# Kernel optimization log

Hardware: AMD Instinct MI355X
Metric: run time of the kernel (lower is better)

## Reference

```python
import jax, jax.numpy as jnp
import numpy as np

EPS = 1e-7  # K.epsilon()


def setup_inputs() -> dict:
    key = jax.random.key(0)
    k1, k2, k3, k4 = jax.random.split(key, 4)
    B, T, S = 512, 32, 2048  # batch, time_steps, seq_len
    inputs = jax.random.normal(k1, (B, T, S), dtype=jnp.float32)
    # Keras mask (float 0/1), same shape as inputs
    mask = (jax.random.uniform(k2, (B, T, S)) < 0.8).astype(jnp.float32)
    # 'uniform' keras initializer: U(-0.05, 0.05)
    W = jax.random.uniform(k3, (S, T, T), minval=-0.05, maxval=0.05, dtype=jnp.float32)
    b = jax.random.uniform(k4, (S, T), minval=-0.05, maxval=0.05, dtype=jnp.float32)
    return {"inputs": inputs, "mask": mask, "W": W, "b": b}


def reference(inputs, mask, W, b):
    # (B,T,S) -> (B,S,T), apply mask
    x = jnp.transpose(inputs, (0, 2, 1)) * jnp.transpose(mask, (0, 2, 1))
    # per-position matmul, batched over B and S (replaces the tf.scan over batch)
    z = jnp.einsum('bst,stu->bsu', x, W) + b  # (B,S,T)
    e = jnp.exp(jnp.tanh(z))
    att = e / (jnp.sum(e, axis=2, keepdims=True) + EPS)  # softmax-like over T
    return jnp.sum(att * x, axis=1)  # (B,T)
```

## Files before the change

### kernel.cpp

```cpp
#include <hip/hip_runtime.h>

#define EPS_K 1e-7f

typedef __attribute__((ext_vector_type(8)))  short          frag8;
typedef __attribute__((ext_vector_type(16))) float          accf16;
typedef __attribute__((ext_vector_type(4)))  unsigned short us4;

__device__ __forceinline__ unsigned f2bf(float f) {
  union { float f; unsigned u; } v; v.f = f;
  unsigned u = v.u;
  u += 0x7FFFu + ((u >> 16) & 1u);
  return u >> 16;
}
__device__ __forceinline__ float bf2f(unsigned short s) {
  union { unsigned u; float f; } v; v.u = ((unsigned)s) << 16;
  return v.f;
}
__device__ __forceinline__ unsigned pk_bf16(float lo, float hi) {
  return f2bf(lo) | (f2bf(hi) << 16);
}

__global__ __launch_bounds__(256) void wbf_prep(
    const float* __restrict__ Wt, unsigned short* __restrict__ Wbf)
{
  __shared__ unsigned short tile[32 * 33];
  const int s   = blockIdx.x;
  const int tid = threadIdx.x;
  {
    const int t  = tid >> 3;
    const int uc = tid & 7;
    const float4 v = *(const float4*)(Wt + s * 1024 + t * 32 + 4 * uc);
    tile[t * 33 + 4 * uc + 0] = (unsigned short)f2bf(v.x);
    tile[t * 33 + 4 * uc + 1] = (unsigned short)f2bf(v.y);
    tile[t * 33 + 4 * uc + 2] = (unsigned short)f2bf(v.z);
    tile[t * 33 + 4 * uc + 3] = (unsigned short)f2bf(v.w);
  }
  __syncthreads();
  {
    const int u  = tid >> 3;
    const int tc = tid & 7;
    uint2 d;
    d.x = (unsigned)tile[(4 * tc + 0) * 33 + u] | ((unsigned)tile[(4 * tc + 1) * 33 + u] << 16);
    d.y = (unsigned)tile[(4 * tc + 2) * 33 + u] | ((unsigned)tile[(4 * tc + 3) * 33 + u] << 16);
    *(uint2*)(Wbf + s * 1024 + u * 32 + 4 * tc) = d;
  }
}

template <bool WBF, bool USE_WS>
__global__ __launch_bounds__(512, 8) void attn_fused(
    const float* __restrict__ inp,
    const float* __restrict__ msk,
    const float* __restrict__ Wt,
    const unsigned short* __restrict__ Wbf,
    const float* __restrict__ bias,
    float* __restrict__ part,
    float* __restrict__ out)
{
  __shared__ unsigned short x_us[32 * 512];

  const int tid = threadIdx.x;
  const int st  = blockIdx.x >> 4;
  const int bg  = blockIdx.x & 15;
  const int s0  = st * 16;

  {
    const int sc = tid & 3;
    const int tb = (tid >> 2) & 3;
    const int b  = tid >> 4;
    const float* ip = inp + ((size_t)(bg * 32 + b) * 32 + 8 * tb) * 2048 + s0 + 4 * sc;
    const float* mp = msk + ((size_t)(bg * 32 + b) * 32 + 8 * tb) * 2048 + s0 + 4 * sc;
    unsigned c32[4][4];
    #pragma unroll
    for (int j2 = 0; j2 < 4; ++j2) {
      const float4 vi0 = *(const float4*)(ip + (2 * j2)     * 2048);
      const float4 vm0 = *(const float4*)(mp + (2 * j2)     * 2048);
      const float4 vi1 = *(const float4*)(ip + (2 * j2 + 1) * 2048);
      const float4 vm1 = *(const float4*)(mp + (2 * j2 + 1) * 2048);
      c32[0][j2] = pk_bf16(vi0.x * vm0.x, vi1.x * vm1.x);
      c32[1][j2] = pk_bf16(vi0.y * vm0.y, vi1.y * vm1.y);
      c32[2][j2] = pk_bf16(vi0.z * vm0.z, vi1.z * vm1.z);
      c32[3][j2] = pk_bf16(vi0.w * vm0.w, vi1.w * vm1.w);
    }
    #pragma unroll
    for (int w = 0; w < 4; ++w) {
      const int L = tb * 16 + 4 * sc + w;
      unsigned* dst = (unsigned*)(x_us + b * 512 + ((L ^ (b & 7)) * 8));
      *(uint4*)dst = make_uint4(c32[w][0], c32[w][1], c32[w][2], c32[w][3]);
    }
  }
  __syncthreads();

  const int lane = tid & 63;
  const int wv   = tid >> 6;
  const int n    = lane & 31;
  const int h    = lane >> 5;
  const int nx   = n & 7;

  float O[16];
  #pragma unroll
  for (int r = 0; r < 16; ++r) O[r] = 0.f;

  #pragma unroll
  for (int si = 0; si < 2; ++si) {
    const int sl = wv * 2 + si;
    const int s  = s0 + sl;

    frag8 a1, a2;
    if (WBF) {
      const unsigned short* wp = Wbf + s * 1024 + n * 32 + 8 * h;
      a1 = *(const frag8*)(wp);
      a2 = *(const frag8*)(wp + 16);
    } else {
      const float* Wp = Wt + s * 1024;
      #pragma unroll
      for (int j = 0; j < 8; ++j) {
        const int t1 = 8 * h + j;
        a1[j] = (short)f2bf(Wp[t1 * 32 + n]);
        a2[j] = (short)f2bf(Wp[(t1 + 16) * 32 + n]);
      }
    }

    const frag8 b1 = *(const frag8*)(x_us + n * 512 + (((h      * 16 + sl) ^ nx) * 8));
    const frag8 b2 = *(const frag8*)(x_us + n * 512 + ((((h + 2) * 16 + sl) ^ nx) * 8));

    accf16 acc;
    #pragma unroll
    for (int g = 0; g < 4; ++g) {
      const float4 bb = *(const float4*)(bias + s * 32 + 8 * g + 4 * h);
      acc[4 * g + 0] = bb.x; acc[4 * g + 1] = bb.y;
      acc[4 * g + 2] = bb.z; acc[4 * g + 3] = bb.w;
    }
    acc = __builtin_amdgcn_mfma_f32_32x32x16_bf16(a1, b1, acc, 0, 0, 0);
    acc = __builtin_amdgcn_mfma_f32_32x32x16_bf16(a2, b2, acc, 0, 0, 0);

    float e[16];
    float ps = 0.f;
    #pragma unroll
    for (int r = 0; r < 16; ++r) {
      const float z  = acc[r];
      const float e2 = __expf(2.f * z);
      const float th = 1.f - 2.f / (e2 + 1.f);
      e[r] = __expf(th);
      ps  += e[r];
    }
    const float tot = ps + __shfl_xor(ps, 32, 64);
    const float inv = 1.f / (tot + EPS_K);

    #pragma unroll
    for (int g = 0; g < 4; ++g) {
      const us4 xv = *(const us4*)(x_us + n * 512 + (((g * 16 + sl) ^ nx) * 8) + 4 * h);
      #pragma unroll
      for (int i = 0; i < 4; ++i)
        O[4 * g + i] += e[4 * g + i] * inv * bf2f(xv[i]);
    }
  }

  __syncthreads();
  float* red = (float*)x_us;
  #pragma unroll
  for (int r = 0; r < 16; ++r) {
    const int u = (r & 3) + 8 * (r >> 2) + 4 * h;
    red[wv * 1024 + n * 32 + (u ^ n)] = O[r];
  }
  __syncthreads();

  const int q0 = tid * 2;
  float2 v;
  #pragma unroll
  for (int i = 0; i < 2; ++i) {
    const int q = q0 + i;
    const int b = q >> 5, u = q & 31;
    float sum = 0.f;
    #pragma unroll
    for (int w = 0; w < 8; ++w) sum += red[w * 1024 + b * 32 + (u ^ b)];
    (&v.x)[i] = sum;
  }
  if (USE_WS) {
    *(float2*)(part + (size_t)st * 16384 + bg * 1024 + q0) = v;
  } else {
    float* op = out + bg * 1024 + q0;
    atomicAdd(op + 0, v.x);
    atomicAdd(op + 1, v.y);
  }
}

__global__ __launch_bounds__(256) void reduce_part(
    const float* __restrict__ part, float* __restrict__ out)
{
  const int f = blockIdx.x * 256 + threadIdx.x;
  float s = 0.f;
  #pragma unroll 8
  for (int st = 0; st < 128; ++st) s += part[(size_t)st * 16384 + f];
  out[f] = s;
}

extern "C" void kernel_launch(void* const* d_in, const int* in_sizes, int n_in,
                              void* d_out, int out_size, void* d_ws, size_t ws_size,
                              hipStream_t stream) {
  const float* inp  = (const float*)d_in[0];
  const float* msk  = (const float*)d_in[1];
  const float* Wt   = (const float*)d_in[2];
  const float* bias = (const float*)d_in[3];
  float* out = (float*)d_out;

  const size_t part_sz = (size_t)128 * 16384 * sizeof(float);
  const size_t wbf_sz  = (size_t)2048 * 1024 * sizeof(unsigned short);

  if (ws_size >= part_sz + wbf_sz) {
    float* part = (float*)d_ws;
    unsigned short* Wbf = (unsigned short*)((char*)d_ws + part_sz);
    wbf_prep<<<dim3(2048), dim3(256), 0, stream>>>(Wt, Wbf);
    attn_fused<true, true><<<dim3(2048), dim3(512), 0, stream>>>(
        inp, msk, Wt, Wbf, bias, part, out);
    reduce_part<<<dim3(64), dim3(256), 0, stream>>>(part, out);
  } else if (ws_size >= part_sz) {
    float* part = (float*)d_ws;
    attn_fused<false, true><<<dim3(2048), dim3(512), 0, stream>>>(
        inp, msk, Wt, nullptr, bias, part, out);
    reduce_part<<<dim3(64), dim3(256), 0, stream>>>(part, out);
  } else {
    (void)hipMemsetAsync(out, 0, (size_t)out_size * sizeof(float), stream);
    attn_fused<false, false><<<dim3(2048), dim3(512), 0, stream>>>(
        inp, msk, Wt, nullptr, bias, nullptr, out);
  }
}
```

Baseline: 335.2 us.

## Make attention kernel persistent over s-chunks with double-buffered LDS prefetch

Each block now handles 8 chunks of 8 sequence positions, strided by 256, instead of one 16-position chunk. Global loads for the next chunk are issued into registers while the current chunk's MFMA and softmax run, and a double-buffered LDS tile replaces the single-shot load. The grid shrinks to 512 blocks, and the partial-sum buffer and its reduction drop from 128 to 32 slices. Divides are swapped for hardware reciprocal, and launch bounds are relaxed to 4 blocks per CU. In exchange there is a strided access pattern across s, fewer blocks to cover latency, and slightly lower reciprocal accuracy.

New measurement: 395.0 us. +17.8%, slower.

```diff
diff --git a/kernel.cpp b/kernel.cpp
--- a/kernel.cpp
+++ b/kernel.cpp
@@ -18,6 +18,9 @@
 }
 __device__ __forceinline__ unsigned pk_bf16(float lo, float hi) {
   return f2bf(lo) | (f2bf(hi) << 16);
+}
+__device__ __forceinline__ float rcp_f(float x) {
+  return __builtin_amdgcn_rcpf(x);
 }
 
 __global__ __launch_bounds__(256) void wbf_prep(
@@ -47,7 +50,7 @@
 }
 
 template <bool WBF, bool USE_WS>
-__global__ __launch_bounds__(512, 8) void attn_fused(
+__global__ __launch_bounds__(512, 4) void attn_fused(
     const float* __restrict__ inp,
     const float* __restrict__ msk,
     const float* __restrict__ Wt,
@@ -56,39 +59,48 @@
     float* __restrict__ part,
     float* __restrict__ out)
 {
-  __shared__ unsigned short x_us[32 * 512];
+  __shared__ unsigned short x_us[2][32 * 256];
 
   const int tid = threadIdx.x;
-  const int st  = blockIdx.x >> 4;
+  const int sq  = blockIdx.x >> 4;
   const int bg  = blockIdx.x & 15;
-  const int s0  = st * 16;
-
-  {
-    const int sc = tid & 3;
-    const int tb = (tid >> 2) & 3;
-    const int b  = tid >> 4;
-    const float* ip = inp + ((size_t)(bg * 32 + b) * 32 + 8 * tb) * 2048 + s0 + 4 * sc;
-    const float* mp = msk + ((size_t)(bg * 32 + b) * 32 + 8 * tb) * 2048 + s0 + 4 * sc;
-    unsigned c32[4][4];
-    #pragma unroll
-    for (int j2 = 0; j2 < 4; ++j2) {
-      const float4 vi0 = *(const float4*)(ip + (2 * j2)     * 2048);
-      const float4 vm0 = *(const float4*)(mp + (2 * j2)     * 2048);
-      const float4 vi1 = *(const float4*)(ip + (2 * j2 + 1) * 2048);
-      const float4 vm1 = *(const float4*)(mp + (2 * j2 + 1) * 2048);
-      c32[0][j2] = pk_bf16(vi0.x * vm0.x, vi1.x * vm1.x);
-      c32[1][j2] = pk_bf16(vi0.y * vm0.y, vi1.y * vm1.y);
-      c32[2][j2] = pk_bf16(vi0.z * vm0.z, vi1.z * vm1.z);
-      c32[3][j2] = pk_bf16(vi0.w * vm0.w, vi1.w * vm1.w);
-    }
-    #pragma unroll
-    for (int w = 0; w < 4; ++w) {
-      const int L = tb * 16 + 4 * sc + w;
-      unsigned* dst = (unsigned*)(x_us + b * 512 + ((L ^ (b & 7)) * 8));
-      *(uint4*)dst = make_uint4(c32[w][0], c32[w][1], c32[w][2], c32[w][3]);
-    }
-  }
-  __syncthreads();
+
+  const int b_s  = tid & 31;
+  const int sc_s = (tid >> 5) & 1;
+  const int tq_s = tid >> 6;
+  const float* ip0 = inp + ((size_t)(bg * 32 + b_s) * 32 + 4 * tq_s) * 2048 + sq * 8 + 4 * sc_s;
+  const float* mp0 = msk + ((size_t)(bg * 32 + b_s) * 32 + 4 * tq_s) * 2048 + sq * 8 + 4 * sc_s;
+
+  float4 vi0, vi1, vi2, vi3, vm0, vm1, vm2, vm3;
+
+#define STAGE_LOAD(k) do {                                                   \
+    const float* ip = ip0 + (k) * 256;                                       \
+    const float* mp = mp0 + (k) * 256;                                       \
+    vi0 = *(const float4*)(ip);          vm0 = *(const float4*)(mp);         \
+    vi1 = *(const float4*)(ip + 2048);   vm1 = *(const float4*)(mp + 2048);  \
+    vi2 = *(const float4*)(ip + 4096);   vm2 = *(const float4*)(mp + 4096);  \
+    vi3 = *(const float4*)(ip + 6144);   vm3 = *(const float4*)(mp + 6144);  \
+  } while (0)
+
+#define STAGE_WRITE(k) do {                                                  \
+    unsigned short* xb = &x_us[(k) & 1][0];                                  \
+    _Pragma("unroll")                                                        \
+    for (int w = 0; w < 4; ++w) {                                            \
+      const int L = (tq_s >> 1) * 8 + 4 * sc_s + w;                          \
+      uint2 d;                                                               \
+      d.x = pk_bf16(((const float*)&vi0)[w] * ((const float*)&vm0)[w],       \
+                    ((const float*)&vi1)[w] * ((const float*)&vm1)[w]);      \
+      d.y = pk_bf16(((const float*)&vi2)[w] * ((const float*)&vm2)[w],       \
+                    ((const float*)&vi3)[w] * ((const float*)&vm3)[w]);      \
+      *(uint2*)(xb + b_s * 256 + ((L ^ (b_s & 7)) * 8) + 4 * (tq_s & 1)) = d;\
+    }                                                                        \
+  } while (0)
+
+#define SYNC do {                                                            \
+    asm volatile("s_waitcnt lgkmcnt(0)" ::: "memory");                       \
+    __builtin_amdgcn_s_barrier();                                            \
+    asm volatile("" ::: "memory");                                           \
+  } while (0)
 
   const int lane = tid & 63;
   const int wv   = tid >> 6;
@@ -100,10 +112,15 @@
   #pragma unroll
   for (int r = 0; r < 16; ++r) O[r] = 0.f;
 
-  #pragma unroll
-  for (int si = 0; si < 2; ++si) {
-    const int sl = wv * 2 + si;
-    const int s  = s0 + sl;
+  STAGE_LOAD(0);
+  STAGE_WRITE(0);
+  STAGE_LOAD(1);
+  SYNC;
+
+  #pragma unroll
+  for (int k = 0; k < 8; ++k) {
+    const int s = k * 256 + sq * 8 + wv;
+    const unsigned short* xb = &x_us[k & 1][0];
 
     frag8 a1, a2;
     if (WBF) {
@@ -120,8 +137,8 @@
       }
     }
 
-    const frag8 b1 = *(const frag8*)(x_us + n * 512 + (((h      * 16 + sl) ^ nx) * 8));
-    const frag8 b2 = *(const frag8*)(x_us + n * 512 + ((((h + 2) * 16 + sl) ^ nx) * 8));
+    const frag8 b1 = *(const frag8*)(xb + n * 256 + (((h      * 8 + wv) ^ nx) * 8));
+    const frag8 b2 = *(const frag8*)(xb + n * 256 + ((((h + 2) * 8 + wv) ^ nx) * 8));
 
     accf16 acc;
     #pragma unroll
@@ -133,30 +150,35 @@
     acc = __builtin_amdgcn_mfma_f32_32x32x16_bf16(a1, b1, acc, 0, 0, 0);
     acc = __builtin_amdgcn_mfma_f32_32x32x16_bf16(a2, b2, acc, 0, 0, 0);
 
-    float e[16];
     float ps = 0.f;
     #pragma unroll
     for (int r = 0; r < 16; ++r) {
       const float z  = acc[r];
       const float e2 = __expf(2.f * z);
-      const float th = 1.f - 2.f / (e2 + 1.f);
-      e[r] = __expf(th);
-      ps  += e[r];
+      const float th = 1.f - 2.f * rcp_f(e2 + 1.f);
+      acc[r] = __expf(th);
+      ps    += acc[r];
     }
     const float tot = ps + __shfl_xor(ps, 32, 64);
-    const float inv = 1.f / (tot + EPS_K);
+    const float inv = rcp_f(tot + EPS_K);
 
     #pragma unroll
     for (int g = 0; g < 4; ++g) {
-      const us4 xv = *(const us4*)(x_us + n * 512 + (((g * 16 + sl) ^ nx) * 8) + 4 * h);
+      const us4 xv = *(const us4*)(xb + n * 256 + (((g * 8 + wv) ^ nx) * 8) + 4 * h);
       #pragma unroll
       for (int i = 0; i < 4; ++i)
-        O[4 * g + i] += e[4 * g + i] * inv * bf2f(xv[i]);
+        O[4 * g + i] += acc[4 * g + i] * inv * bf2f(xv[i]);
+    }
+
+    if (k < 7) {
+      STAGE_WRITE(k + 1);
+      if (k < 6) STAGE_LOAD(k + 2);
+      SYNC;
     }
   }
 
   __syncthreads();
-  float* red = (float*)x_us;
+  float* red = (float*)&x_us[0][0];
   #pragma unroll
   for (int r = 0; r < 16; ++r) {
     const int u = (r & 3) + 8 * (r >> 2) + 4 * h;
@@ -176,12 +198,16 @@
     (&v.x)[i] = sum;
   }
   if (USE_WS) {
-    *(float2*)(part + (size_t)st * 16384 + bg * 1024 + q0) = v;
+    *(float2*)(part + (size_t)sq * 16384 + bg * 1024 + q0) = v;
   } else {
     float* op = out + bg * 1024 + q0;
     atomicAdd(op + 0, v.x);
     atomicAdd(op + 1, v.y);
   }
+
+#undef STAGE_LOAD
+#undef STAGE_WRITE
+#undef SYNC
 }
 
 __global__ __launch_bounds__(256) void reduce_part(
@@ -190,7 +216,7 @@
   const int f = blockIdx.x * 256 + threadIdx.x;
   float s = 0.f;
   #pragma unroll 8
-  for (int st = 0; st < 128; ++st) s += part[(size_t)st * 16384 + f];
+  for (int sq = 0; sq < 32; ++sq) s += part[(size_t)sq * 16384 + f];
   out[f] = s;
 }
 
@@ -203,24 +229,24 @@
   const float* bias = (const float*)d_in[3];
   float* out = (float*)d_out;
 
-  const size_t part_sz = (size_t)128 * 16384 * sizeof(float);
+  const size_t part_sz = (size_t)32 * 16384 * sizeof(float);
   const size_t wbf_sz  = (size_t)2048 * 1024 * sizeof(unsigned short);
 
   if (ws_size >= part_sz + wbf_sz) {
     float* part = (float*)d_ws;
     unsigned short* Wbf = (unsigned short*)((char*)d_ws + part_sz);
     wbf_prep<<<dim3(2048), dim3(256), 0, stream>>>(Wt, Wbf);
-    attn_fused<true, true><<<dim3(2048), dim3(512), 0, stream>>>(
+    attn_fused<true, true><<<dim3(512), dim3(512), 0, stream>>>(
         inp, msk, Wt, Wbf, bias, part, out);
     reduce_part<<<dim3(64), dim3(256), 0, stream>>>(part, out);
   } else if (ws_size >= part_sz) {
     float* part = (float*)d_ws;
-    attn_fused<false, true><<<dim3(2048), dim3(512), 0, stream>>>(
+    attn_fused<false, true><<<dim3(512), dim3(512), 0, stream>>>(
         inp, msk, Wt, nullptr, bias, part, out);
     reduce_part<<<dim3(64), dim3(256), 0, stream>>>(part, out);
   } else {
     (void)hipMemsetAsync(out, 0, (size_t)out_size * sizeof(float), stream);
-    attn_fused<false, false><<<dim3(2048), dim3(512), 0, stream>>>(
+    attn_fused<false, false><<<dim3(512), dim3(512), 0, stream>>>(
         inp, msk, Wt, nullptr, bias, nullptr, out);
   }
 }
```
